# Performance work log

Measured on AMD Instinct MI355X. Metric: run time of the kernel, lower is better.

## Reference

```python
import jax, jax.numpy as jnp
import numpy as np

N = 50000          # nodes
E = 800000         # edges (avg degree 16)
INPUT_DIM = 1024
K = 10             # conv1d kernel
STRIDE = 8
COUT = (INPUT_DIM - K) // STRIDE + 1   # 127, matches floor formula
H = 256            # hidden_dim


def setup_inputs() -> dict:
    key = jax.random.key(0)
    ks = jax.random.split(key, 12)
    sc = lambda k, s: (jax.random.normal(k, s, jnp.float32) * 0.05)
    inp = {}
    inp["h"] = jax.random.normal(ks[0], (N, INPUT_DIM), jnp.float32)
    inp["src"] = jax.random.randint(ks[1], (E,), 0, N, dtype=jnp.int32)
    inp["dst"] = jax.random.randint(ks[2], (E,), 0, N, dtype=jnp.int32)
    # Conv1d(1,1,k=10,stride=8)
    inp["conv1d_w"] = sc(ks[3], (1, 1, K))
    inp["conv1d_b"] = jnp.zeros((1,), jnp.float32)
    # SAGEConv1: 127 -> 256 (mean aggregator: fc_self + fc_neigh)
    inp["w_self1"] = sc(ks[4], (COUT, H))
    inp["w_neigh1"] = sc(ks[5], (COUT, H))
    inp["b1"] = jnp.zeros((H,), jnp.float32)
    # SAGEConv2: 256 -> 128
    inp["w_self2"] = sc(ks[6], (H, H // 2))
    inp["w_neigh2"] = sc(ks[7], (H, H // 2))
    inp["b2"] = jnp.zeros((H // 2,), jnp.float32)
    # MLP head 128 -> 64 -> 32 -> 1
    inp["fc1_w"] = sc(ks[8], (H // 2, H // 4)); inp["fc1_b"] = jnp.zeros((H // 4,), jnp.float32)
    inp["fc2_w"] = sc(ks[9], (H // 4, H // 8)); inp["fc2_b"] = jnp.zeros((H // 8,), jnp.float32)
    inp["fc3_w"] = sc(ks[10], (H // 8, 1));    inp["fc3_b"] = jnp.zeros((1,), jnp.float32)
    return inp


def _sage_mean(x, src, dst, w_self, w_neigh, b):
    # mean over in-neighbors (src -> dst), zero for isolated nodes (DGL semantics)
    ones = jnp.ones((src.shape[0],), x.dtype)
    deg = jax.ops.segment_sum(ones, dst, num_segments=N)          # [N]
    agg = jax.ops.segment_sum(x[src], dst, num_segments=N)        # [N, F]
    agg = agg / jnp.maximum(deg, 1.0)[:, None]
    return x @ w_self + agg @ w_neigh + b


def reference(h, src, dst, conv1d_w, conv1d_b,
              w_self1, w_neigh1, b1, w_self2, w_neigh2, b2,
              fc1_w, fc1_b, fc2_w, fc2_b, fc3_w, fc3_b):
    # per-node 1D conv over feature axis: [N,1,1024] -> [N,1,127]
    x = jax.lax.conv_general_dilated(h[:, None, :], conv1d_w, (STRIDE,), 'VALID',
                                     dimension_numbers=('NCH', 'OIH', 'NCH'))
    x = jax.nn.relu(x[:, 0, :] + conv1d_b)                        # [N, 127]
    x = jax.nn.relu(_sage_mean(x, src, dst, w_self1, w_neigh1, b1))  # [N, 256]
    x = jax.nn.relu(_sage_mean(x, src, dst, w_self2, w_neigh2, b2))  # [N, 128]
    hg = jnp.mean(x, axis=0, keepdims=True)                       # AvgPooling -> [1, 128]
    y = jax.nn.relu(hg @ fc1_w + fc1_b)
    y = jax.nn.relu(y @ fc2_w + fc2_b)
    return y @ fc3_w + fc3_b                                      # [1, 1]
```

## Files before the change

### kernel.cpp

```cpp
#include <hip/hip_runtime.h>

#define N_NODES 50000
#define N_EDGES 800000
#define IN_DIM  1024
#define COUT    127
#define H1      256
#define H2      128
#define LDA     256
#define MBLK    391
#define EPB     2048
#define NROWS   8192
#define LDSS    72

typedef __bf16 bf16;
typedef __attribute__((ext_vector_type(8))) __bf16 bf16x8;
typedef __attribute__((ext_vector_type(2))) __bf16 bf16x2;
typedef __attribute__((ext_vector_type(4))) float floatx4;

__device__ __forceinline__ float blo(unsigned int u) { return __uint_as_float(u << 16); }
__device__ __forceinline__ float bhi(unsigned int u) { return __uint_as_float(u & 0xffff0000u); }

__global__ __launch_bounds__(256) void conv_kernel(const float* __restrict__ h,
                                                   const float* __restrict__ w,
                                                   const float* __restrict__ b,
                                                   bf16* __restrict__ xa) {
    int t    = threadIdx.x & 127;
    int half = threadIdx.x >> 7;
    float wv[10];
    #pragma unroll
    for (int j = 0; j < 10; ++j) wv[j] = w[j];
    float bb = b[0];
    for (int n = blockIdx.x * 2 + half; n < N_NODES; n += gridDim.x * 2) {
        const float* hr = h + (size_t)n * IN_DIM;
        float r = 0.f;
        if (t < COUT) {
            const float* p = hr + t * 8;
            float4 a = *(const float4*)p;
            float4 c = *(const float4*)(p + 4);
            float2 d = *(const float2*)(p + 8);
            float s = bb;
            s += a.x * wv[0] + a.y * wv[1] + a.z * wv[2] + a.w * wv[3];
            s += c.x * wv[4] + c.y * wv[5] + c.z * wv[6] + c.w * wv[7];
            s += d.x * wv[8] + d.y * wv[9];
            r = fmaxf(s, 0.f);
        }
        xa[(size_t)n * LDA + t] = (bf16)r;
    }
}

__global__ void padw_kernel(const float* __restrict__ ws1, const float* __restrict__ wn1,
                            const float* __restrict__ ws2, const float* __restrict__ wn2,
                            bf16* __restrict__ wt1, bf16* __restrict__ wt2,
                            int* __restrict__ deg) {
    int i = blockIdx.x * blockDim.x + threadIdx.x;
    int j = i & 65535;
    int n = j >> 8, k = j & 255;
    if (i < 65536) {
        float v = 0.f;
        if (k < COUT)                        v = ws1[k * H1 + n];
        else if (k >= 128 && k < 128 + COUT) v = wn1[(k - 128) * H1 + n];
        wt1[j] = (bf16)v;
    } else {
        float v = (n < H2) ? ws2[k * H2 + n] : wn2[k * H2 + (n - H2)];
        wt2[j] = (bf16)v;
    }
    if (i < 50048) deg[i] = 0;
}

__global__ void deg_kernel(const int* __restrict__ dst, int* __restrict__ deg) {
    int e = blockIdx.x * blockDim.x + threadIdx.x;
    if (e < N_EDGES) atomicAdd(&deg[dst[e]], 1);
}

__global__ __launch_bounds__(1024) void scan_kernel(const int* __restrict__ deg,
                                                    int* __restrict__ rowptr,
                                                    int* __restrict__ cursor) {
    __shared__ int wsum[16];
    __shared__ int carry_s;
    int tid = threadIdx.x;
    int lane = tid & 63, wid = tid >> 6;
    if (tid == 0) carry_s = 0;
    __syncthreads();
    for (int base = 0; base < N_NODES; base += 8192) {
        int i0 = base + tid * 8;
        int v[8];
        if (i0 + 8 <= N_NODES) {
            int4 a = *(const int4*)&deg[i0];
            int4 c = *(const int4*)&deg[i0 + 4];
            v[0] = a.x; v[1] = a.y; v[2] = a.z; v[3] = a.w;
            v[4] = c.x; v[5] = c.y; v[6] = c.z; v[7] = c.w;
        } else {
            #pragma unroll
            for (int j = 0; j < 8; ++j) v[j] = (i0 + j < N_NODES) ? deg[i0 + j] : 0;
        }
        int p[8]; int run = 0;
        #pragma unroll
        for (int j = 0; j < 8; ++j) { run += v[j]; p[j] = run; }
        int s = run;
        #pragma unroll
        for (int off = 1; off < 64; off <<= 1) {
            int t = __shfl_up(s, off);
            if (lane >= off) s += t;
        }
        if (lane == 63) wsum[wid] = s;
        __syncthreads();
        if (tid < 16) {
            int ws = wsum[tid];
            #pragma unroll
            for (int off = 1; off < 16; off <<= 1) {
                int t = __shfl_up(ws, off);
                if (tid >= off) ws += t;
            }
            wsum[tid] = ws;
        }
        __syncthreads();
        int wpre  = (wid == 0) ? 0 : wsum[wid - 1];
        int excl0 = carry_s + wpre + (s - run);
        int o[8];
        #pragma unroll
        for (int j = 0; j < 8; ++j) o[j] = excl0 + p[j] - v[j];
        if (i0 + 8 <= N_NODES) {
            *(int4*)&rowptr[i0]     = make_int4(o[0], o[1], o[2], o[3]);
            *(int4*)&rowptr[i0 + 4] = make_int4(o[4], o[5], o[6], o[7]);
            *(int4*)&cursor[i0]     = make_int4(o[0], o[1], o[2], o[3]);
            *(int4*)&cursor[i0 + 4] = make_int4(o[4], o[5], o[6], o[7]);
        } else {
            for (int j = 0; j < 8; ++j)
                if (i0 + j < N_NODES) { rowptr[i0 + j] = o[j]; cursor[i0 + j] = o[j]; }
        }
        int tot = wsum[15];
        __syncthreads();
        if (tid == 0) carry_s += tot;
        __syncthreads();
    }
    if (tid == 0) rowptr[N_NODES] = carry_s;
}

__global__ void fill_kernel(const int* __restrict__ src, const int* __restrict__ dst,
                            int* __restrict__ cursor, int* __restrict__ esrc) {
    int e = blockIdx.x * blockDim.x + threadIdx.x;
    if (e < N_EDGES) {
        int d = dst[e];
        int pos = atomicAdd(&cursor[d], 1);
        esrc[pos] = src[e];
    }
}

__global__ __launch_bounds__(256) void agg_kernel(bf16* __restrict__ xa,
                                                  const int* __restrict__ rowptr,
                                                  const int* __restrict__ esrc) {
    int lane = threadIdx.x & 63;
    int w    = threadIdx.x >> 6;
    int n    = blockIdx.x * 4 + w;
    int s0 = __builtin_amdgcn_readfirstlane(rowptr[n]);
    int s1 = __builtin_amdgcn_readfirstlane(rowptr[n + 1]);
    float ax = 0.f, ay = 0.f;
    int e = s0;
    for (; e + 8 <= s1; e += 8) {
        int i0 = esrc[e],     i1 = esrc[e + 1], i2 = esrc[e + 2], i3 = esrc[e + 3];
        int i4 = esrc[e + 4], i5 = esrc[e + 5], i6 = esrc[e + 6], i7 = esrc[e + 7];
        unsigned u0 = ((const unsigned*)(xa + (size_t)i0 * LDA))[lane];
        unsigned u1 = ((const unsigned*)(xa + (size_t)i1 * LDA))[lane];
        unsigned u2 = ((const unsigned*)(xa + (size_t)i2 * LDA))[lane];
        unsigned u3 = ((const unsigned*)(xa + (size_t)i3 * LDA))[lane];
        unsigned u4 = ((const unsigned*)(xa + (size_t)i4 * LDA))[lane];
        unsigned u5 = ((const unsigned*)(xa + (size_t)i5 * LDA))[lane];
        unsigned u6 = ((const unsigned*)(xa + (size_t)i6 * LDA))[lane];
        unsigned u7 = ((const unsigned*)(xa + (size_t)i7 * LDA))[lane];
        ax += ((blo(u0) + blo(u1)) + (blo(u2) + blo(u3)))
            + ((blo(u4) + blo(u5)) + (blo(u6) + blo(u7)));
        ay += ((bhi(u0) + bhi(u1)) + (bhi(u2) + bhi(u3)))
            + ((bhi(u4) + bhi(u5)) + (bhi(u6) + bhi(u7)));
    }
    for (; e < s1; ++e) {
        unsigned u = ((const unsigned*)(xa + (size_t)esrc[e] * LDA))[lane];
        ax += blo(u); ay += bhi(u);
    }
    float dnm = (float)max(s1 - s0, 1);
    bf16x2 o;
    o[0] = (bf16)(ax / dnm);
    o[1] = (bf16)(ay / dnm);
    *(bf16x2*)(xa + (size_t)n * LDA + 128 + 2 * lane) = o;
}

template <bool RELU>
__global__ __launch_bounds__(256) void gemm_mfma(
        const bf16* __restrict__ X, const bf16* __restrict__ WT,
        const float* __restrict__ bias, bf16* __restrict__ out) {
    __shared__ bf16 As[128 * LDSS];
    __shared__ bf16 Bs[64 * LDSS];
    int tid  = threadIdx.x;
    int lane = tid & 63, w = tid >> 6;
    int quad = lane >> 4, l16 = lane & 15;
    int m0 = blockIdx.x * 128;
    int n0 = blockIdx.y * 64;
    floatx4 acc[2][4] = {};

    for (int k0 = 0; k0 < 256; k0 += 64) {
        uint4 av[4], bv[2];
        #pragma unroll
        for (int i = 0; i < 4; ++i) {
            int c = tid + 256 * i;
            int row = c >> 3, col = (c & 7) * 8;
            int gr = m0 + row;
            av[i] = (gr < N_NODES) ? *(const uint4*)(X + (size_t)gr * LDA + k0 + col)
                                   : make_uint4(0u, 0u, 0u, 0u);
        }
        #pragma unroll
        for (int i = 0; i < 2; ++i) {
            int c = tid + 256 * i;
            int row = c >> 3, col = (c & 7) * 8;
            bv[i] = *(const uint4*)(WT + (size_t)(n0 + row) * 256 + k0 + col);
        }
        __syncthreads();
        #pragma unroll
        for (int i = 0; i < 4; ++i) {
            int c = tid + 256 * i;
            int row = c >> 3, col = (c & 7) * 8;
            *(uint4*)&As[row * LDSS + col] = av[i];
        }
        #pragma unroll
        for (int i = 0; i < 2; ++i) {
            int c = tid + 256 * i;
            int row = c >> 3, col = (c & 7) * 8;
            *(uint4*)&Bs[row * LDSS + col] = bv[i];
        }
        __syncthreads();

        #pragma unroll
        for (int ks = 0; ks < 2; ++ks) {
            int kin = ks * 32 + quad * 8;
            bf16x8 a0 = *(const bf16x8*)&As[(w * 32 + l16) * LDSS + kin];
            bf16x8 a1 = *(const bf16x8*)&As[(w * 32 + 16 + l16) * LDSS + kin];
            bf16x8 b0 = *(const bf16x8*)&Bs[(l16) * LDSS + kin];
            bf16x8 b1 = *(const bf16x8*)&Bs[(16 + l16) * LDSS + kin];
            bf16x8 b2 = *(const bf16x8*)&Bs[(32 + l16) * LDSS + kin];
            bf16x8 b3 = *(const bf16x8*)&Bs[(48 + l16) * LDSS + kin];
            acc[0][0] = __builtin_amdgcn_mfma_f32_16x16x32_bf16(a0, b0, acc[0][0], 0, 0, 0);
            acc[0][1] = __builtin_amdgcn_mfma_f32_16x16x32_bf16(a0, b1, acc[0][1], 0, 0, 0);
            acc[0][2] = __builtin_amdgcn_mfma_f32_16x16x32_bf16(a0, b2, acc[0][2], 0, 0, 0);
            acc[0][3] = __builtin_amdgcn_mfma_f32_16x16x32_bf16(a0, b3, acc[0][3], 0, 0, 0);
            acc[1][0] = __builtin_amdgcn_mfma_f32_16x16x32_bf16(a1, b0, acc[1][0], 0, 0, 0);
            acc[1][1] = __builtin_amdgcn_mfma_f32_16x16x32_bf16(a1, b1, acc[1][1], 0, 0, 0);
            acc[1][2] = __builtin_amdgcn_mfma_f32_16x16x32_bf16(a1, b2, acc[1][2], 0, 0, 0);
            acc[1][3] = __builtin_amdgcn_mfma_f32_16x16x32_bf16(a1, b3, acc[1][3], 0, 0, 0);
        }
    }

    float bvv[4] = {};
    if constexpr (RELU) {
        #pragma unroll
        for (int nt = 0; nt < 4; ++nt) bvv[nt] = bias[n0 + nt * 16 + l16];
    }
    #pragma unroll
    for (int mt = 0; mt < 2; ++mt) {
        #pragma unroll
        for (int r = 0; r < 4; ++r) {
            int m = m0 + w * 32 + mt * 16 + quad * 4 + r;
            if (m < N_NODES) {
                #pragma unroll
                for (int nt = 0; nt < 4; ++nt) {
                    float v = acc[mt][nt][r];
                    if constexpr (RELU) v = fmaxf(v + bvv[nt], 0.f);
                    out[(size_t)m * LDA + n0 + nt * 16 + l16] = (bf16)v;
                }
            }
        }
    }
}

__global__ __launch_bounds__(256) void agg_epi_kernel(
        const bf16* __restrict__ P, const int* __restrict__ rowptr,
        const int* __restrict__ esrc, const float* __restrict__ b2,
        float* __restrict__ partial) {
    int lane = threadIdx.x & 63;
    int w    = threadIdx.x >> 6;
    int wid  = blockIdx.x * 4 + w;
    float2 bfv = *(const float2*)(b2 + 2 * lane);
    float csx = 0.f, csy = 0.f;
    for (int n = wid; n < N_NODES; n += 4 * gridDim.x) {
        int s0 = __builtin_amdgcn_readfirstlane(rowptr[n]);
        int s1 = __builtin_amdgcn_readfirstlane(rowptr[n + 1]);
        float ax = 0.f, ay = 0.f;
        int e = s0;
        for (; e + 8 <= s1; e += 8) {
            int i0 = esrc[e],     i1 = esrc[e + 1], i2 = esrc[e + 2], i3 = esrc[e + 3];
            int i4 = esrc[e + 4], i5 = esrc[e + 5], i6 = esrc[e + 6], i7 = esrc[e + 7];
            unsigned u0 = ((const unsigned*)(P + (size_t)i0 * LDA + H2))[lane];
            unsigned u1 = ((const unsigned*)(P + (size_t)i1 * LDA + H2))[lane];
            unsigned u2 = ((const unsigned*)(P + (size_t)i2 * LDA + H2))[lane];
            unsigned u3 = ((const unsigned*)(P + (size_t)i3 * LDA + H2))[lane];
            unsigned u4 = ((const unsigned*)(P + (size_t)i4 * LDA + H2))[lane];
            unsigned u5 = ((const unsigned*)(P + (size_t)i5 * LDA + H2))[lane];
            unsigned u6 = ((const unsigned*)(P + (size_t)i6 * LDA + H2))[lane];
            unsigned u7 = ((const unsigned*)(P + (size_t)i7 * LDA + H2))[lane];
            ax += ((blo(u0) + blo(u1)) + (blo(u2) + blo(u3)))
                + ((blo(u4) + blo(u5)) + (blo(u6) + blo(u7)));
            ay += ((bhi(u0) + bhi(u1)) + (bhi(u2) + bhi(u3)))
                + ((bhi(u4) + bhi(u5)) + (bhi(u6) + bhi(u7)));
        }
        for (; e < s1; ++e) {
            unsigned u = ((const unsigned*)(P + (size_t)esrc[e] * LDA + H2))[lane];
            ax += blo(u); ay += bhi(u);
        }
        float dnm = (float)max(s1 - s0, 1);
        unsigned us = ((const unsigned*)(P + (size_t)n * LDA))[lane];
        float yx = blo(us) + ax / dnm + bfv.x;
        float yy = bhi(us) + ay / dnm + bfv.y;
        csx += fmaxf(yx, 0.f);
        csy += fmaxf(yy, 0.f);
    }
    *(float2*)(partial + (size_t)wid * 128 + 2 * lane) = make_float2(csx, csy);
}

__global__ __launch_bounds__(256) void reduce_kernel(const float* __restrict__ partial,
                                                     float* __restrict__ hg) {
    int f = blockIdx.x, t = threadIdx.x;
    float s = 0.f;
    for (int i = t; i < NROWS; i += 256) s += partial[(size_t)i * 128 + f];
    __shared__ float ls[4];
    #pragma unroll
    for (int off = 32; off >= 1; off >>= 1) s += __shfl_down(s, off);
    if ((t & 63) == 0) ls[t >> 6] = s;
    __syncthreads();
    if (t == 0) hg[f] = (ls[0] + ls[1]) + (ls[2] + ls[3]);
}

__global__ void mlp_kernel(const float* __restrict__ hg,
                           const float* __restrict__ f1w, const float* __restrict__ f1b,
                           const float* __restrict__ f2w, const float* __restrict__ f2b,
                           const float* __restrict__ f3w, const float* __restrict__ f3b,
                           float* __restrict__ out) {
    __shared__ float h0[128], y1[64], y2[32];
    int t = threadIdx.x;
    if (t < 128) h0[t] = hg[t] * (1.0f / N_NODES);
    __syncthreads();
    if (t < 64) {
        float s = f1b[t];
        for (int k = 0; k < 128; ++k) s += h0[k] * f1w[k * 64 + t];
        y1[t] = fmaxf(s, 0.f);
    }
    __syncthreads();
    if (t < 32) {
        float s = f2b[t];
        for (int k = 0; k < 64; ++k) s += y1[k] * f2w[k * 32 + t];
        y2[t] = fmaxf(s, 0.f);
    }
    __syncthreads();
    if (t == 0) {
        float s = f3b[0];
        for (int k = 0; k < 32; ++k) s += y2[k] * f3w[k];
        out[0] = s;
    }
}

extern "C" void kernel_launch(void* const* d_in, const int* in_sizes, int n_in,
                              void* d_out, int out_size, void* d_ws, size_t ws_size,
                              hipStream_t stream) {
    (void)in_sizes; (void)n_in; (void)out_size; (void)ws_size;
    const float* h        = (const float*)d_in[0];
    const int*   src      = (const int*)d_in[1];
    const int*   dst      = (const int*)d_in[2];
    const float* cw       = (const float*)d_in[3];
    const float* cb       = (const float*)d_in[4];
    const float* w_self1  = (const float*)d_in[5];
    const float* w_neigh1 = (const float*)d_in[6];
    const float* b1       = (const float*)d_in[7];
    const float* w_self2  = (const float*)d_in[8];
    const float* w_neigh2 = (const float*)d_in[9];
    const float* b2       = (const float*)d_in[10];
    const float* f1w      = (const float*)d_in[11];
    const float* f1b      = (const float*)d_in[12];
    const float* f2w      = (const float*)d_in[13];
    const float* f2b      = (const float*)d_in[14];
    const float* f3w      = (const float*)d_in[15];
    const float* f3b      = (const float*)d_in[16];
    float* out = (float*)d_out;

    char* ws = (char*)d_ws;
    bf16*  xa    = (bf16*) (ws + 0);
    bf16*  P     = (bf16*) (ws + 0);
    bf16*  x2    = (bf16*) (ws + 25624576);
    bf16*  wt1   = (bf16*) (ws + 51249152);
    bf16*  wt2   = (bf16*) (ws + 51380224);
    int*   deg   = (int*)  (ws + 51511296);
    int*   rowp  = (int*)  (ws + 51711488);
    int*   esrc  = (int*)  (ws + 51911936);
    float* part  = (float*)(ws + 55111936);
    float* hg    = (float*)(ws + 59306240);
    int*   cur   = deg;

    padw_kernel<<<512, 256, 0, stream>>>(w_self1, w_neigh1, w_self2, w_neigh2, wt1, wt2, deg);
    deg_kernel<<<(N_EDGES + 255) / 256, 256, 0, stream>>>(dst, deg);
    scan_kernel<<<1, 1024, 0, stream>>>(deg, rowp, cur);
    fill_kernel<<<(N_EDGES + 255) / 256, 256, 0, stream>>>(src, dst, cur, esrc);
    conv_kernel<<<2048, 256, 0, stream>>>(h, cw, cb, xa);
    agg_kernel<<<12500, 256, 0, stream>>>(xa, rowp, esrc);
    dim3 g(MBLK, 4);
    gemm_mfma<true><<<g, 256, 0, stream>>>(xa, wt1, b1, x2);
    gemm_mfma<false><<<g, 256, 0, stream>>>(x2, wt2, nullptr, P);
    agg_epi_kernel<<<EPB, 256, 0, stream>>>(P, rowp, esrc, b2, part);
    reduce_kernel<<<128, 256, 0, stream>>>(part, hg);
    mlp_kernel<<<1, 128, 0, stream>>>(hg, f1w, f1b, f2w, f2b, f3w, f3b, out);
}
```

Before: 553.1 us.

## Overlap conv1d with degree counting and scan by co-launching in shared kernels

The conv1d work is split into two halves, and each half is fused into the same launch as the degree-count atomics and the single-block prefix scan, using disjoint block ranges. This hides the latency-bound, one-block scan and the atomic degree pass behind the bandwidth-heavy conv read of h, and removes one kernel launch. Blocks are now 1024 threads. The conv blocks may compete with the scan block for resources, and each conv block now covers eight nodes per iteration.

```diff
diff --git a/kernel.cpp b/kernel.cpp
--- a/kernel.cpp
+++ b/kernel.cpp
@@ -11,6 +11,8 @@
 #define EPB     2048
 #define NROWS   8192
 #define LDSS    72
+#define EBLK    782
+#define CVB     256
 
 typedef __bf16 bf16;
 typedef __attribute__((ext_vector_type(8))) __bf16 bf16x8;
@@ -20,24 +22,23 @@
 __device__ __forceinline__ float blo(unsigned int u) { return __uint_as_float(u << 16); }
 __device__ __forceinline__ float bhi(unsigned int u) { return __uint_as_float(u & 0xffff0000u); }
 
-__global__ __launch_bounds__(256) void conv_kernel(const float* __restrict__ h,
-                                                   const float* __restrict__ w,
-                                                   const float* __restrict__ b,
-                                                   bf16* __restrict__ xa) {
-    int t    = threadIdx.x & 127;
-    int half = threadIdx.x >> 7;
+__device__ __forceinline__ void conv_range(const float* __restrict__ h,
+                                           const float* __restrict__ w, float bb,
+                                           bf16* __restrict__ xa,
+                                           int lo, int hi, int cb, int ncb) {
+    int t   = threadIdx.x & 127;
+    int sub = threadIdx.x >> 7;
     float wv[10];
     #pragma unroll
     for (int j = 0; j < 10; ++j) wv[j] = w[j];
-    float bb = b[0];
-    for (int n = blockIdx.x * 2 + half; n < N_NODES; n += gridDim.x * 2) {
+    for (int n = lo + cb * 8 + sub; n < hi; n += ncb * 8) {
         const float* hr = h + (size_t)n * IN_DIM;
         float r = 0.f;
         if (t < COUT) {
-            const float* p = hr + t * 8;
-            float4 a = *(const float4*)p;
-            float4 c = *(const float4*)(p + 4);
-            float2 d = *(const float2*)(p + 8);
+            const float* q = hr + t * 8;
+            float4 a = *(const float4*)q;
+            float4 c = *(const float4*)(q + 4);
+            float2 d = *(const float2*)(q + 8);
             float s = bb;
             s += a.x * wv[0] + a.y * wv[1] + a.z * wv[2] + a.w * wv[3];
             s += c.x * wv[4] + c.y * wv[5] + c.z * wv[6] + c.w * wv[7];
@@ -67,14 +68,21 @@
     if (i < 50048) deg[i] = 0;
 }
 
-__global__ void deg_kernel(const int* __restrict__ dst, int* __restrict__ deg) {
-    int e = blockIdx.x * blockDim.x + threadIdx.x;
-    if (e < N_EDGES) atomicAdd(&deg[dst[e]], 1);
-}
-
-__global__ __launch_bounds__(1024) void scan_kernel(const int* __restrict__ deg,
-                                                    int* __restrict__ rowptr,
-                                                    int* __restrict__ cursor) {
+__global__ __launch_bounds__(1024) void deg_conv_kernel(
+        const int* __restrict__ dst, int* __restrict__ deg,
+        const float* __restrict__ h, const float* __restrict__ cw,
+        const float* __restrict__ cb, bf16* __restrict__ xa) {
+    int bid = blockIdx.x;
+    if (bid < EBLK) {
+        int e = bid * 1024 + threadIdx.x;
+        if (e < N_EDGES) atomicAdd(&deg[dst[e]], 1);
+    } else {
+        conv_range(h, cw, cb[0], xa, 0, 25000, bid - EBLK, CVB);
+    }
+}
+
+__device__ void scan_block(const int* __restrict__ deg, int* __restrict__ rowptr,
+                           int* __restrict__ cursor) {
     __shared__ int wsum[16];
     __shared__ int carry_s;
     int tid = threadIdx.x;
@@ -136,9 +144,21 @@
     if (tid == 0) rowptr[N_NODES] = carry_s;
 }
 
-__global__ void fill_kernel(const int* __restrict__ src, const int* __restrict__ dst,
-                            int* __restrict__ cursor, int* __restrict__ esrc) {
-    int e = blockIdx.x * blockDim.x + threadIdx.x;
+__global__ __launch_bounds__(1024) void scan_conv_kernel(
+        const int* __restrict__ deg, int* __restrict__ rowptr, int* __restrict__ cursor,
+        const float* __restrict__ h, const float* __restrict__ cw,
+        const float* __restrict__ cb, bf16* __restrict__ xa) {
+    if (blockIdx.x == 0) {
+        scan_block(deg, rowptr, cursor);
+    } else {
+        conv_range(h, cw, cb[0], xa, 25000, N_NODES, blockIdx.x - 1, CVB);
+    }
+}
+
+__global__ __launch_bounds__(1024) void fill_kernel(
+        const int* __restrict__ src, const int* __restrict__ dst,
+        int* __restrict__ cursor, int* __restrict__ esrc) {
+    int e = blockIdx.x * 1024 + threadIdx.x;
     if (e < N_EDGES) {
         int d = dst[e];
         int pos = atomicAdd(&cursor[d], 1);
@@ -391,10 +411,9 @@
     int*   cur   = deg;
 
     padw_kernel<<<512, 256, 0, stream>>>(w_self1, w_neigh1, w_self2, w_neigh2, wt1, wt2, deg);
-    deg_kernel<<<(N_EDGES + 255) / 256, 256, 0, stream>>>(dst, deg);
-    scan_kernel<<<1, 1024, 0, stream>>>(deg, rowp, cur);
-    fill_kernel<<<(N_EDGES + 255) / 256, 256, 0, stream>>>(src, dst, cur, esrc);
-    conv_kernel<<<2048, 256, 0, stream>>>(h, cw, cb, xa);
+    deg_conv_kernel<<<EBLK + CVB, 1024, 0, stream>>>(dst, deg, h, cw, cb, xa);
+    scan_conv_kernel<<<1 + CVB, 1024, 0, stream>>>(deg, rowp, cur, h, cw, cb, xa);
+    fill_kernel<<<EBLK, 1024, 0, stream>>>(src, dst, cur, esrc);
     agg_kernel<<<12500, 256, 0, stream>>>(xa, rowp, esrc);
     dim3 g(MBLK, 4);
     gemm_mfma<true><<<g, 256, 0, stream>>>(xa, wt1, b1, x2);
```

Result: faster. 538.0 us (-2.7%).
